# Optimization experiments

Hardware: AMD Instinct MI355X
Metric: run time of the kernel (lower is better)

Reference implementation:

```python
import jax, jax.numpy as jnp
import numpy as np

N = 100000      # nodes
E = 600000      # directed edges (reciprocal pairs)
D_NODE = 128    # node feature dim (== hidden, required by torch.where broadcast)
D_BOND = 16     # bond feature dim
HID = 128       # hidden size
DEPTH = 3       # message passing depth


def setup_inputs() -> dict:
    key = jax.random.key(0)
    ks = jax.random.split(key, 8)
    x = jax.random.normal(ks[0], (N, D_NODE), jnp.float32)
    # build edges as reciprocal pairs: edge 2i = (u,v), edge 2i+1 = (v,u)
    half = E // 2
    u = jax.random.randint(ks[1], (half,), 0, N)
    v = jax.random.randint(ks[2], (half,), 0, N)
    src = jnp.stack([u, v], axis=1).reshape(-1)
    dst = jnp.stack([v, u], axis=1).reshape(-1)
    edge_index = jnp.stack([src, dst])          # [2, E]
    rev_edge_index = jnp.arange(E) ^ 1           # reverse edge of 2i is 2i+1
    edge_attr = jax.random.normal(ks[3], (E, D_BOND), jnp.float32)
    # learned params (Linear: y = x @ W + b)
    s_i = 1.0 / np.sqrt(D_NODE + D_BOND)
    s_h = 1.0 / np.sqrt(HID)
    s_o = 1.0 / np.sqrt(D_NODE + HID)
    W_i = jax.random.normal(ks[4], (D_NODE + D_BOND, HID), jnp.float32) * s_i
    b_i = jnp.zeros((HID,), jnp.float32)
    W_h = jax.random.normal(ks[5], (HID, HID), jnp.float32) * s_h
    b_h = jnp.zeros((HID,), jnp.float32)
    W_o = jax.random.normal(ks[6], (D_NODE + HID, HID), jnp.float32) * s_o
    b_o = jnp.zeros((HID,), jnp.float32)
    return dict(x=x, edge_attr=edge_attr, W_i=W_i, b_i=b_i, W_h=W_h, b_h=b_h,
                W_o=W_o, b_o=b_o, edge_index=edge_index,
                rev_edge_index=rev_edge_index)


def reference(x, edge_attr, W_i, b_i, W_h, b_h, W_o, b_o,
              edge_index, rev_edge_index):
    src, dst = edge_index[0], edge_index[1]
    # H_0 = relu(W_i([x[src]; edge_attr]))
    H0 = jax.nn.relu(jnp.concatenate([x[src], edge_attr], axis=1) @ W_i + b_i)
    H = H0
    for _ in range(DEPTH - 1):
        # message: scatter-sum over dst, gather by src, subtract reverse edge
        agg = jax.ops.segment_sum(H, dst, num_segments=N)   # [N, HID]
        M = agg[src] - H[rev_edge_index]                    # [E, HID]
        # update: relu(H0 + W_h(M))   (dropout is identity in eval)
        H = jax.nn.relu(H0 + M @ W_h + b_h)
    # final node aggregation
    Mn = jax.ops.segment_sum(H, dst, num_segments=N)        # [N, HID]
    Mn = jnp.where(jnp.sum(Mn, axis=1, keepdims=True) == 0, x, Mn)
    out = jax.nn.relu(jnp.concatenate([x, Mn], axis=1) @ W_o + b_o)  # [N, HID]
    return out
```

## Files before the change

kernel.cpp:

```cpp
#include <hip/hip_runtime.h>
#include <hip/hip_bf16.h>

#define N_NODES 100000
#define N_EDGES 600000
#define HID 128
#define D_BOND 16
#define NB_CHUNKS 98

typedef __attribute__((ext_vector_type(8))) short bf16x8;
typedef __attribute__((ext_vector_type(4))) float f32x4;

__device__ __forceinline__ float bf2f(unsigned int u) {
    return __uint_as_float((u & 0xffffu) << 16);
}
__device__ __forceinline__ unsigned short f2bf(float f) {
    unsigned int x = __float_as_uint(f);
    x += 0x7fffu + ((x >> 16) & 1u);
    return (unsigned short)(x >> 16);
}
__device__ __forceinline__ unsigned int pk2(float a, float b) {
    return (unsigned int)f2bf(a) | ((unsigned int)f2bf(b) << 16);
}

__device__ __forceinline__ void st16(unsigned char* tile, int row, int u, uint4 v) {
    *reinterpret_cast<uint4*>(tile + ((row * 512 + u * 16) ^ ((row & 7) << 4))) = v;
}
__device__ __forceinline__ uint4 ld16(const unsigned char* tile, int row, int u) {
    return *reinterpret_cast<const uint4*>(tile + ((row * 512 + u * 16) ^ ((row & 7) << 4)));
}
__device__ __forceinline__ bf16x8 ld_a(const unsigned char* tile, int row, int kbyte) {
    return *reinterpret_cast<const bf16x8*>(tile + ((row * 512 + kbyte) ^ ((row & 7) << 4)));
}
__device__ __forceinline__ void st2(unsigned char* tile, int row, int col, unsigned short v) {
    *reinterpret_cast<unsigned short*>(tile + ((row * 512 + col * 2) ^ ((row & 7) << 4))) = v;
}

template<int NK>
__device__ __forceinline__ void gemm_frag(const unsigned char* tile, const unsigned short* Wp,
                                          int wr, int cb, int l, f32x4 (&acc)[4]) {
    const int arow = 16 * wr + (l & 15);
    const int abyte0 = (l >> 4) * 16;
#pragma unroll
    for (int kk = 0; kk < NK; ++kk) {
        const bf16x8 a = ld_a(tile, arow, kk * 64 + abyte0);
#pragma unroll
        for (int c = 0; c < 4; ++c) {
            const bf16x8 b = *reinterpret_cast<const bf16x8*>(&Wp[(((kk * 8) + cb + c) * 64 + l) * 8]);
            acc[c] = __builtin_amdgcn_mfma_f32_16x16x32_bf16(a, b, acc[c], 0, 0, 0);
        }
    }
}

template<int NK>
__device__ __forceinline__ void gemm_frag2(const unsigned char* tile, const unsigned short* Wp,
                                           int wr0, int cb, int l, f32x4 (&acc)[2][4]) {
    const int abyte0 = (l >> 4) * 16;
    const int ar0 = 16 * wr0 + (l & 15);
#pragma unroll
    for (int kk = 0; kk < NK; ++kk) {
        const bf16x8 a0 = ld_a(tile, ar0, kk * 64 + abyte0);
        const bf16x8 a1 = ld_a(tile, ar0 + 16, kk * 64 + abyte0);
#pragma unroll
        for (int c = 0; c < 4; ++c) {
            const bf16x8 b = *reinterpret_cast<const bf16x8*>(&Wp[(((kk * 8) + cb + c) * 64 + l) * 8]);
            acc[0][c] = __builtin_amdgcn_mfma_f32_16x16x32_bf16(a0, b, acc[0][c], 0, 0, 0);
            acc[1][c] = __builtin_amdgcn_mfma_f32_16x16x32_bf16(a1, b, acc[1][c], 0, 0, 0);
        }
    }
}

__device__ __forceinline__ void epilogue_store(unsigned char* tile,
                                               f32x4 (&acc)[2][4],
                                               const float* __restrict__ bias,
                                               unsigned short* __restrict__ Hdst,
                                               int e0, int wr0, int cb, int l, int t) {
#pragma unroll
    for (int r = 0; r < 2; ++r) {
        const int rbase = 16 * (wr0 + r) + 4 * (l >> 4);
#pragma unroll
        for (int c = 0; c < 4; ++c) {
            const int col = ((cb + c) << 4) | (l & 15);
            const float bv = bias[col];
#pragma unroll
            for (int rr = 0; rr < 4; ++rr)
                st2(tile, rbase + rr, col, f2bf(fmaxf(acc[r][c][rr] + bv, 0.f)));
        }
    }
    __syncthreads();
#pragma unroll
    for (int i = 0; i < 4; ++i) {
        const int f = t + 256 * i;
        const int row = f >> 4, u = f & 15;
        *reinterpret_cast<uint4*>(&Hdst[(size_t)(e0 + row) * HID + u * 8]) = ld16(tile, row, u);
    }
}

__global__ __launch_bounds__(256) void k_hist(const int* __restrict__ dst,
                                              int* __restrict__ cnt) {
    int e = blockIdx.x * 256 + threadIdx.x;
    if (e < N_EDGES) atomicAdd(&cnt[dst[e]], 1);
}

__global__ __launch_bounds__(256) void k_blocksum(const int* __restrict__ cnt,
                                                  int* __restrict__ bsum) {
    __shared__ int red[256];
    const int b = blockIdx.x, t = threadIdx.x;
    const int base = b * 1024 + t * 4;
    int s = 0;
#pragma unroll
    for (int i = 0; i < 4; ++i) { int n = base + i; if (n < N_NODES) s += cnt[n]; }
    red[t] = s; __syncthreads();
    for (int o = 128; o > 0; o >>= 1) { if (t < o) red[t] += red[t + o]; __syncthreads(); }
    if (t == 0) bsum[b] = red[0];
}

__global__ __launch_bounds__(128) void k_scan_bsum(const int* __restrict__ bsum,
                                                   int* __restrict__ boff,
                                                   int* __restrict__ rowptr) {
    __shared__ int s[128];
    const int t = threadIdx.x;
    const int v = (t < NB_CHUNKS) ? bsum[t] : 0;
    s[t] = v; __syncthreads();
    for (int o = 1; o < 128; o <<= 1) {
        int add = 0; if (t >= o) add = s[t - o];
        __syncthreads();
        s[t] += add; __syncthreads();
    }
    if (t < NB_CHUNKS) boff[t] = s[t] - v;
    if (t == 0) rowptr[N_NODES] = N_EDGES;
}

__global__ __launch_bounds__(256) void k_scan_chunk(const int* __restrict__ cnt,
                                                    const int* __restrict__ boff,
                                                    int* __restrict__ rowptr,
                                                    int* __restrict__ wpos) {
    __shared__ int s[256];
    const int b = blockIdx.x, t = threadIdx.x;
    const int base = b * 1024 + t * 4;
    int v[4]; int ts = 0;
#pragma unroll
    for (int i = 0; i < 4; ++i) { int n = base + i; v[i] = (n < N_NODES) ? cnt[n] : 0; ts += v[i]; }
    s[t] = ts; __syncthreads();
    for (int o = 1; o < 256; o <<= 1) {
        int add = 0; if (t >= o) add = s[t - o];
        __syncthreads();
        s[t] += add; __syncthreads();
    }
    int run = s[t] - ts + boff[b];
#pragma unroll
    for (int i = 0; i < 4; ++i) {
        int n = base + i;
        if (n < N_NODES) { rowptr[n] = run; wpos[n] = run; }
        run += v[i];
    }
}

__global__ __launch_bounds__(256) void k_fill(const int* __restrict__ dst,
                                              int* __restrict__ wpos,
                                              int* __restrict__ eidx) {
    int e = blockIdx.x * 256 + threadIdx.x;
    if (e < N_EDGES) { int p = atomicAdd(&wpos[dst[e]], 1); eidx[p] = e; }
}

__global__ __launch_bounds__(256) void k_xcvt(const float* __restrict__ x,
                                              unsigned short* __restrict__ xbf) {
    const size_t i = (size_t)(blockIdx.x * 256 + threadIdx.x) * 8;
    const float4 v0 = *reinterpret_cast<const float4*>(&x[i]);
    const float4 v1 = *reinterpret_cast<const float4*>(&x[i + 4]);
    uint4 o;
    o.x = pk2(v0.x, v0.y); o.y = pk2(v0.z, v0.w);
    o.z = pk2(v1.x, v1.y); o.w = pk2(v1.z, v1.w);
    *reinterpret_cast<uint4*>(&xbf[i]) = o;
}

__global__ __launch_bounds__(256) void k_pack(const float* __restrict__ Wi,
                                              const float* __restrict__ Wh,
                                              const float* __restrict__ Wo,
                                              unsigned short* __restrict__ Pi,
                                              unsigned short* __restrict__ Ph,
                                              unsigned short* __restrict__ PhN,
                                              unsigned short* __restrict__ Po) {
    const int tid = blockIdx.x * 256 + threadIdx.x;
    const float* W; unsigned short* P; int Krows, base; float sgn = 1.f;
    if (tid < 2560)      { W = Wi; P = Pi;  Krows = 144; base = tid; }
    else if (tid < 4608) { W = Wh; P = Ph;  Krows = 128; base = tid - 2560; }
    else if (tid < 6656) { W = Wh; P = PhN; Krows = 128; base = tid - 4608; sgn = -1.f; }
    else                 { W = Wo; P = Po;  Krows = 256; base = tid - 6656; }
    const int l = base & 63, fc = base >> 6;
    const int c = fc & 7, kk = fc >> 3;
    const int col = c * 16 + (l & 15);
    const int k0 = kk * 32 + (l >> 4) * 8;
    float v[8];
#pragma unroll
    for (int j = 0; j < 8; ++j) {
        const int k = k0 + j;
        v[j] = (k < Krows) ? sgn * W[(size_t)k * HID + col] : 0.f;
    }
    uint4 o;
    o.x = pk2(v[0], v[1]); o.y = pk2(v[2], v[3]);
    o.z = pk2(v[4], v[5]); o.w = pk2(v[6], v[7]);
    *reinterpret_cast<uint4*>(&P[(size_t)base * 8]) = o;
}

__device__ __forceinline__ void stage_xe64(unsigned char* tile, const unsigned short* __restrict__ xbf,
                                           const float* __restrict__ ea, const int* s_src,
                                           int e0, int t) {
#pragma unroll
    for (int f = t; f < 1024; f += 256) {
        const int e = f >> 4, u = f & 15;
        const uint4 v = *reinterpret_cast<const uint4*>(&xbf[(size_t)s_src[e] * HID + u * 8]);
        st16(tile, e, u, v);
    }
    if (t < 128) {
        const int e = t >> 1, u = t & 1;
        const float* ep = &ea[(size_t)(e0 + e) * D_BOND + u * 8];
        const float4 v0 = *reinterpret_cast<const float4*>(ep);
        const float4 v1 = *reinterpret_cast<const float4*>(ep + 4);
        uint4 o;
        o.x = pk2(v0.x, v0.y); o.y = pk2(v0.z, v0.w);
        o.z = pk2(v1.x, v1.y); o.w = pk2(v1.z, v1.w);
        st16(tile, e, 16 + u, o);
    } else {
        const int i = t - 128, e = i >> 1, u = i & 1;
        st16(tile, e, 18 + u, make_uint4(0, 0, 0, 0));
    }
}

__global__ __launch_bounds__(256) void k_h0(const unsigned short* __restrict__ xbf,
                                            const float* __restrict__ ea,
                                            const unsigned short* __restrict__ Pi,
                                            const float* __restrict__ bi,
                                            const int* __restrict__ src,
                                            unsigned short* __restrict__ H) {
    __shared__ __align__(16) unsigned char tile[64 * 512];
    __shared__ int s_src[64];
    const int e0 = blockIdx.x * 64;
    const int t = threadIdx.x;
    if (t < 64) s_src[t] = src[e0 + t];
    __syncthreads();
    stage_xe64(tile, xbf, ea, s_src, e0, t);
    __syncthreads();
    const int w = t >> 6, l = t & 63;
    const int cb = (w & 1) * 4, wr0 = (w >> 1) * 2;
    f32x4 acc[2][4] = {};
    gemm_frag2<5>(tile, Pi, wr0, cb, l, acc);
    __syncthreads();
    epilogue_store(tile, acc, bi, H, e0, wr0, cb, l, t);
}

__global__ __launch_bounds__(256) void k_agg(const unsigned short* __restrict__ H,
                                             const int* __restrict__ rowptr,
                                             const int* __restrict__ eidx,
                                             void* __restrict__ aggv) {
    const int wid = (blockIdx.x * 256 + threadIdx.x) >> 6;
    const int lane = threadIdx.x & 63;
    if (wid >= N_NODES) return;
    const int beg = rowptr[wid], end = rowptr[wid + 1];
    float a0 = 0.f, a1 = 0.f;
    int j = beg;
    for (; j + 4 <= end; j += 4) {
        const int ei0 = eidx[j], ei1 = eidx[j + 1], ei2 = eidx[j + 2], ei3 = eidx[j + 3];
        const unsigned int p0 = *reinterpret_cast<const unsigned int*>(&H[(size_t)ei0 * HID + lane * 2]);
        const unsigned int p1 = *reinterpret_cast<const unsigned int*>(&H[(size_t)ei1 * HID + lane * 2]);
        const unsigned int p2 = *reinterpret_cast<const unsigned int*>(&H[(size_t)ei2 * HID + lane * 2]);
        const unsigned int p3 = *reinterpret_cast<const unsigned int*>(&H[(size_t)ei3 * HID + lane * 2]);
        a0 += bf2f(p0) + bf2f(p1) + bf2f(p2) + bf2f(p3);
        a1 += bf2f(p0 >> 16) + bf2f(p1 >> 16) + bf2f(p2 >> 16) + bf2f(p3 >> 16);
    }
    for (; j < end; ++j) {
        const int e = eidx[j];
        const unsigned int p = *reinterpret_cast<const unsigned int*>(&H[(size_t)e * HID + lane * 2]);
        a0 += bf2f(p);
        a1 += bf2f(p >> 16);
    }
    *reinterpret_cast<unsigned int*>((char*)aggv + (size_t)wid * 512 + lane * 4) = pk2(a0, a1);
}

__global__ __launch_bounds__(256) void k_msg(const unsigned short* __restrict__ xbf,
                                             const float* __restrict__ ea,
                                             const void* __restrict__ aggv,
                                             const unsigned short* __restrict__ Pi,
                                             const float* __restrict__ bi,
                                             const unsigned short* __restrict__ Ph,
                                             const unsigned short* __restrict__ PhN,
                                             const float* __restrict__ bh,
                                             const int* __restrict__ src,
                                             unsigned short* H) {
    __shared__ __align__(16) unsigned char tile[64 * 512];
    __shared__ int s_src[64];
    const int e0 = blockIdx.x * 64;
    const int t = threadIdx.x;
    if (t < 64) s_src[t] = src[e0 + t];
    __syncthreads();
    const int w = t >> 6, l = t & 63;
    const int cb = (w & 1) * 4, wr0 = (w >> 1) * 2;

    stage_xe64(tile, xbf, ea, s_src, e0, t);
    __syncthreads();
    f32x4 acc[2][4] = {};
    gemm_frag2<5>(tile, Pi, wr0, cb, l, acc);
#pragma unroll
    for (int r = 0; r < 2; ++r)
#pragma unroll
        for (int c = 0; c < 4; ++c) {
            const float bv = bi[((cb + c) << 4) | (l & 15)];
#pragma unroll
            for (int rr = 0; rr < 4; ++rr) acc[r][c][rr] = fmaxf(acc[r][c][rr] + bv, 0.f);
        }
    __syncthreads();

#pragma unroll
    for (int f = t; f < 1024; f += 256) {
        const int e = f >> 4, u = f & 15;
        st16(tile, e, u,
             *reinterpret_cast<const uint4*>((const char*)aggv + (size_t)s_src[e] * 512 + u * 16));
    }
    __syncthreads();
    gemm_frag2<4>(tile, Ph, wr0, cb, l, acc);
    __syncthreads();

#pragma unroll
    for (int f = t; f < 1024; f += 256) {
        const int e = f >> 4, u = f & 15;
        st16(tile, e, u,
             *reinterpret_cast<const uint4*>(&H[(size_t)((e0 + e) ^ 1) * HID + u * 8]));
    }
    __syncthreads();
    gemm_frag2<4>(tile, PhN, wr0, cb, l, acc);
    __syncthreads();

    epilogue_store(tile, acc, bh, H, e0, wr0, cb, l, t);
}

__global__ __launch_bounds__(256) void k_out(const float* __restrict__ x,
                                             const void* aggv,
                                             const int* __restrict__ cnt,
                                             const unsigned short* __restrict__ Po,
                                             const float* __restrict__ bo,
                                             float* out) {
    __shared__ __align__(16) unsigned char tile[32 * 512];
    __shared__ int s_cnt[32];
    const int n0 = blockIdx.x * 32;
    const int t = threadIdx.x;
    if (t < 32) s_cnt[t] = cnt[n0 + t];
    __syncthreads();
    for (int f = t; f < 1024; f += 256) {
        const int e = f >> 5, u = f & 31;
        uint4 o;
        if (u >= 16 && s_cnt[e] > 0) {
            o = *reinterpret_cast<const uint4*>((const char*)aggv + (size_t)(n0 + e) * 512 + (u - 16) * 16);
        } else {
            const int k8 = (u & 15) * 8;
            const float* xp = &x[(size_t)(n0 + e) * HID + k8];
            const float4 v0 = *reinterpret_cast<const float4*>(xp);
            const float4 v1 = *reinterpret_cast<const float4*>(xp + 4);
            o.x = pk2(v0.x, v0.y); o.y = pk2(v0.z, v0.w);
            o.z = pk2(v1.x, v1.y); o.w = pk2(v1.z, v1.w);
        }
        st16(tile, e, u, o);
    }
    __syncthreads();
    const int w = t >> 6, l = t & 63;
    const int wr = w & 1, cb = (w >> 1) * 4;
    f32x4 acc[4] = {};
    gemm_frag<8>(tile, Po, wr, cb, l, acc);
    const int frow = 16 * wr + 4 * (l >> 4);
#pragma unroll
    for (int c = 0; c < 4; ++c) {
        const int col = ((cb + c) << 4) | (l & 15);
        const float bias = bo[col];
#pragma unroll
        for (int r = 0; r < 4; ++r) {
            out[(size_t)(n0 + frow + r) * HID + col] = fmaxf(acc[c][r] + bias, 0.f);
        }
    }
}

extern "C" void kernel_launch(void* const* d_in, const int* in_sizes, int n_in,
                              void* d_out, int out_size, void* d_ws, size_t ws_size,
                              hipStream_t stream) {
    const float* x  = (const float*)d_in[0];
    const float* ea = (const float*)d_in[1];
    const float* Wi = (const float*)d_in[2];
    const float* bi = (const float*)d_in[3];
    const float* Wh = (const float*)d_in[4];
    const float* bh = (const float*)d_in[5];
    const float* Wo = (const float*)d_in[6];
    const float* bo = (const float*)d_in[7];
    const int* ei   = (const int*)d_in[8];
    const int* src  = ei;
    const int* dst  = ei + N_EDGES;

    char* ws = (char*)d_ws;
    size_t off = 0;
    auto alloc = [&](size_t bytes) -> void* {
        void* p = ws + off;
        off += (bytes + 255) & ~(size_t)255;
        return p;
    };
    unsigned short* H  = (unsigned short*)alloc((size_t)N_EDGES * HID * 2);
    unsigned short* xbf = (unsigned short*)alloc((size_t)N_NODES * HID * 2);
    int* cnt     = (int*)alloc((size_t)N_NODES * 4);
    int* rowptr  = (int*)alloc((size_t)(N_NODES + 1) * 4);
    int* wpos    = (int*)alloc((size_t)N_NODES * 4);
    int* bsum    = (int*)alloc(512);
    int* boff    = (int*)alloc(512);
    int* eidx    = (int*)alloc((size_t)N_EDGES * 4);
    unsigned short* Pi  = (unsigned short*)alloc(2560 * 8 * 2);
    unsigned short* Ph  = (unsigned short*)alloc(2048 * 8 * 2);
    unsigned short* PhN = (unsigned short*)alloc(2048 * 8 * 2);
    unsigned short* Po  = (unsigned short*)alloc(4096 * 8 * 2);
    void* agg = d_out;

    const int EB = (N_EDGES + 255) / 256;

    hipMemsetAsync(cnt, 0, (size_t)N_NODES * 4, stream);
    k_hist<<<EB, 256, 0, stream>>>(dst, cnt);
    k_blocksum<<<NB_CHUNKS, 256, 0, stream>>>(cnt, bsum);
    k_scan_bsum<<<1, 128, 0, stream>>>(bsum, boff, rowptr);
    k_scan_chunk<<<NB_CHUNKS, 256, 0, stream>>>(cnt, boff, rowptr, wpos);
    k_fill<<<EB, 256, 0, stream>>>(dst, wpos, eidx);

    k_xcvt<<<6250, 256, 0, stream>>>(x, xbf);
    k_pack<<<42, 256, 0, stream>>>(Wi, Wh, Wo, Pi, Ph, PhN, Po);

    k_h0<<<N_EDGES / 64, 256, 0, stream>>>(xbf, ea, Pi, bi, src, H);

    k_agg<<<N_NODES / 4, 256, 0, stream>>>(H, rowptr, eidx, agg);
    k_msg<<<N_EDGES / 64, 256, 0, stream>>>(xbf, ea, agg, Pi, bi, Ph, PhN, bh, src, H);

    k_agg<<<N_NODES / 4, 256, 0, stream>>>(H, rowptr, eidx, agg);
    k_msg<<<N_EDGES / 64, 256, 0, stream>>>(xbf, ea, agg, Pi, bi, Ph, PhN, bh, src, H);

    k_agg<<<N_NODES / 4, 256, 0, stream>>>(H, rowptr, eidx, agg);
    k_out<<<N_NODES / 32, 256, 0, stream>>>(x, agg, cnt, Po, bo, (float*)d_out);
}
```

Before: 685.6 us.

## Precompute per-node x@W_i and interleave with aggregate for single gather per edge

Instead of gathering bf16 x per edge and running a K=144 GEMM for H0 in every edge kernel, a new node-level kernel computes x@W_i[:128] once per node and stores it in bf16 alongside the aggregate in one 512-byte row. The edge kernels then gather that combined row once. They inject the precomputed projection into the accumulators through identity-matrix MFMAs, and run only a K=16 GEMM for the bond features, which are now pre-converted to bf16. k_msg also stages all operands in one phase rather than three sequential stage/GEMM rounds, cutting barriers at the cost of more shared memory. Rounding x@W_i to bf16 before adding adds a small precision loss.

```diff
diff --git a/kernel.cpp b/kernel.cpp
--- a/kernel.cpp
+++ b/kernel.cpp
@@ -22,77 +22,30 @@
     return (unsigned int)f2bf(a) | ((unsigned int)f2bf(b) << 16);
 }
 
-__device__ __forceinline__ void st16(unsigned char* tile, int row, int u, uint4 v) {
-    *reinterpret_cast<uint4*>(tile + ((row * 512 + u * 16) ^ ((row & 7) << 4))) = v;
-}
-__device__ __forceinline__ uint4 ld16(const unsigned char* tile, int row, int u) {
-    return *reinterpret_cast<const uint4*>(tile + ((row * 512 + u * 16) ^ ((row & 7) << 4)));
-}
-__device__ __forceinline__ bf16x8 ld_a(const unsigned char* tile, int row, int kbyte) {
-    return *reinterpret_cast<const bf16x8*>(tile + ((row * 512 + kbyte) ^ ((row & 7) << 4)));
-}
-__device__ __forceinline__ void st2(unsigned char* tile, int row, int col, unsigned short v) {
-    *reinterpret_cast<unsigned short*>(tile + ((row * 512 + col * 2) ^ ((row & 7) << 4))) = v;
-}
-
-template<int NK>
-__device__ __forceinline__ void gemm_frag(const unsigned char* tile, const unsigned short* Wp,
-                                          int wr, int cb, int l, f32x4 (&acc)[4]) {
-    const int arow = 16 * wr + (l & 15);
-    const int abyte0 = (l >> 4) * 16;
-#pragma unroll
-    for (int kk = 0; kk < NK; ++kk) {
-        const bf16x8 a = ld_a(tile, arow, kk * 64 + abyte0);
-#pragma unroll
-        for (int c = 0; c < 4; ++c) {
-            const bf16x8 b = *reinterpret_cast<const bf16x8*>(&Wp[(((kk * 8) + cb + c) * 64 + l) * 8]);
-            acc[c] = __builtin_amdgcn_mfma_f32_16x16x32_bf16(a, b, acc[c], 0, 0, 0);
-        }
-    }
-}
-
-template<int NK>
-__device__ __forceinline__ void gemm_frag2(const unsigned char* tile, const unsigned short* Wp,
-                                           int wr0, int cb, int l, f32x4 (&acc)[2][4]) {
-    const int abyte0 = (l >> 4) * 16;
-    const int ar0 = 16 * wr0 + (l & 15);
-#pragma unroll
-    for (int kk = 0; kk < NK; ++kk) {
-        const bf16x8 a0 = ld_a(tile, ar0, kk * 64 + abyte0);
-        const bf16x8 a1 = ld_a(tile, ar0 + 16, kk * 64 + abyte0);
-#pragma unroll
-        for (int c = 0; c < 4; ++c) {
-            const bf16x8 b = *reinterpret_cast<const bf16x8*>(&Wp[(((kk * 8) + cb + c) * 64 + l) * 8]);
-            acc[0][c] = __builtin_amdgcn_mfma_f32_16x16x32_bf16(a0, b, acc[0][c], 0, 0, 0);
-            acc[1][c] = __builtin_amdgcn_mfma_f32_16x16x32_bf16(a1, b, acc[1][c], 0, 0, 0);
-        }
-    }
-}
-
-__device__ __forceinline__ void epilogue_store(unsigned char* tile,
-                                               f32x4 (&acc)[2][4],
-                                               const float* __restrict__ bias,
-                                               unsigned short* __restrict__ Hdst,
-                                               int e0, int wr0, int cb, int l, int t) {
-#pragma unroll
-    for (int r = 0; r < 2; ++r) {
-        const int rbase = 16 * (wr0 + r) + 4 * (l >> 4);
-#pragma unroll
-        for (int c = 0; c < 4; ++c) {
-            const int col = ((cb + c) << 4) | (l & 15);
-            const float bv = bias[col];
-#pragma unroll
-            for (int rr = 0; rr < 4; ++rr)
-                st2(tile, rbase + rr, col, f2bf(fmaxf(acc[r][c][rr] + bv, 0.f)));
-        }
-    }
-    __syncthreads();
-#pragma unroll
-    for (int i = 0; i < 4; ++i) {
-        const int f = t + 256 * i;
-        const int row = f >> 4, u = f & 15;
-        *reinterpret_cast<uint4*>(&Hdst[(size_t)(e0 + row) * HID + u * 8]) = ld16(tile, row, u);
-    }
+template<int STRIDE, int XM>
+__device__ __forceinline__ void stw(unsigned char* tile, int row, int byte, uint4 v) {
+    *reinterpret_cast<uint4*>(tile + ((row * STRIDE + byte) ^ ((row & XM) << 4))) = v;
+}
+template<int STRIDE, int XM>
+__device__ __forceinline__ uint4 ldw(const unsigned char* tile, int row, int byte) {
+    return *reinterpret_cast<const uint4*>(tile + ((row * STRIDE + byte) ^ ((row & XM) << 4)));
+}
+template<int STRIDE, int XM>
+__device__ __forceinline__ bf16x8 lda(const unsigned char* tile, int row, int byte) {
+    return *reinterpret_cast<const bf16x8*>(tile + ((row * STRIDE + byte) ^ ((row & XM) << 4)));
+}
+template<int STRIDE, int XM>
+__device__ __forceinline__ void st2w(unsigned char* tile, int row, int col, unsigned short v) {
+    *reinterpret_cast<unsigned short*>(tile + ((row * STRIDE + col * 2) ^ ((row & XM) << 4))) = v;
+}
+
+__device__ __forceinline__ bf16x8 ifrag(int l, int shift) {
+    bf16x8 b;
+    const int target = (l & 15) + shift;
+#pragma unroll
+    for (int j = 0; j < 8; ++j)
+        b[j] = (short)((((l >> 4) * 8 + j) == target) ? 0x3F80 : 0);
+    return b;
 }
 
 __global__ __launch_bounds__(256) void k_hist(const int* __restrict__ dst,
@@ -162,30 +115,33 @@
     if (e < N_EDGES) { int p = atomicAdd(&wpos[dst[e]], 1); eidx[p] = e; }
 }
 
-__global__ __launch_bounds__(256) void k_xcvt(const float* __restrict__ x,
-                                              unsigned short* __restrict__ xbf) {
+__global__ __launch_bounds__(256) void k_eacvt(const float* __restrict__ ea,
+                                               unsigned short* __restrict__ eabf) {
     const size_t i = (size_t)(blockIdx.x * 256 + threadIdx.x) * 8;
-    const float4 v0 = *reinterpret_cast<const float4*>(&x[i]);
-    const float4 v1 = *reinterpret_cast<const float4*>(&x[i + 4]);
+    if (i >= (size_t)N_EDGES * D_BOND) return;
+    const float4 v0 = *reinterpret_cast<const float4*>(&ea[i]);
+    const float4 v1 = *reinterpret_cast<const float4*>(&ea[i + 4]);
     uint4 o;
     o.x = pk2(v0.x, v0.y); o.y = pk2(v0.z, v0.w);
     o.z = pk2(v1.x, v1.y); o.w = pk2(v1.z, v1.w);
-    *reinterpret_cast<uint4*>(&xbf[i]) = o;
+    *reinterpret_cast<uint4*>(&eabf[i]) = o;
 }
 
 __global__ __launch_bounds__(256) void k_pack(const float* __restrict__ Wi,
                                               const float* __restrict__ Wh,
                                               const float* __restrict__ Wo,
-                                              unsigned short* __restrict__ Pi,
+                                              unsigned short* __restrict__ Pie,
+                                              unsigned short* __restrict__ Pix,
                                               unsigned short* __restrict__ Ph,
                                               unsigned short* __restrict__ PhN,
                                               unsigned short* __restrict__ Po) {
     const int tid = blockIdx.x * 256 + threadIdx.x;
     const float* W; unsigned short* P; int Krows, base; float sgn = 1.f;
-    if (tid < 2560)      { W = Wi; P = Pi;  Krows = 144; base = tid; }
-    else if (tid < 4608) { W = Wh; P = Ph;  Krows = 128; base = tid - 2560; }
-    else if (tid < 6656) { W = Wh; P = PhN; Krows = 128; base = tid - 4608; sgn = -1.f; }
-    else                 { W = Wo; P = Po;  Krows = 256; base = tid - 6656; }
+    if (tid < 512)        { W = Wi + 128 * HID; P = Pie; Krows = 16;  base = tid; }
+    else if (tid < 2560)  { W = Wi; P = Pix; Krows = 128; base = tid - 512; }
+    else if (tid < 4608)  { W = Wh; P = Ph;  Krows = 128; base = tid - 2560; }
+    else if (tid < 6656)  { W = Wh; P = PhN; Krows = 128; base = tid - 4608; sgn = -1.f; }
+    else                  { W = Wo; P = Po;  Krows = 256; base = tid - 6656; }
     const int l = base & 63, fc = base >> 6;
     const int c = fc & 7, kk = fc >> 3;
     const int col = c * 16 + (l & 15);
@@ -202,56 +158,138 @@
     *reinterpret_cast<uint4*>(&P[(size_t)base * 8]) = o;
 }
 
-__device__ __forceinline__ void stage_xe64(unsigned char* tile, const unsigned short* __restrict__ xbf,
-                                           const float* __restrict__ ea, const int* s_src,
-                                           int e0, int t) {
-#pragma unroll
-    for (int f = t; f < 1024; f += 256) {
-        const int e = f >> 4, u = f & 15;
-        const uint4 v = *reinterpret_cast<const uint4*>(&xbf[(size_t)s_src[e] * HID + u * 8]);
-        st16(tile, e, u, v);
-    }
-    if (t < 128) {
-        const int e = t >> 1, u = t & 1;
-        const float* ep = &ea[(size_t)(e0 + e) * D_BOND + u * 8];
-        const float4 v0 = *reinterpret_cast<const float4*>(ep);
-        const float4 v1 = *reinterpret_cast<const float4*>(ep + 4);
+__global__ __launch_bounds__(256) void k_xw(const float* __restrict__ x,
+                                            const unsigned short* __restrict__ Pix,
+                                            void* __restrict__ xa) {
+    __shared__ __align__(16) unsigned char tX[32 * 256];
+    const int n0 = blockIdx.x * 32;
+    const int t = threadIdx.x;
+#pragma unroll
+    for (int i = 0; i < 2; ++i) {
+        const int f = t + 256 * i, row = f >> 4, u = f & 15;
+        const float* xp = &x[(size_t)(n0 + row) * HID + u * 8];
+        const float4 v0 = *reinterpret_cast<const float4*>(xp);
+        const float4 v1 = *reinterpret_cast<const float4*>(xp + 4);
         uint4 o;
         o.x = pk2(v0.x, v0.y); o.y = pk2(v0.z, v0.w);
         o.z = pk2(v1.x, v1.y); o.w = pk2(v1.z, v1.w);
-        st16(tile, e, 16 + u, o);
-    } else {
-        const int i = t - 128, e = i >> 1, u = i & 1;
-        st16(tile, e, 18 + u, make_uint4(0, 0, 0, 0));
-    }
-}
-
-__global__ __launch_bounds__(256) void k_h0(const unsigned short* __restrict__ xbf,
-                                            const float* __restrict__ ea,
-                                            const unsigned short* __restrict__ Pi,
+        stw<256, 7>(tX, row, u * 16, o);
+    }
+    __syncthreads();
+    const int w = t >> 6, l = t & 63;
+    const int wr = w & 1, cb = (w >> 1) * 4;
+    const int arow = 16 * wr + (l & 15);
+    const int ko = (l >> 4) * 16;
+    f32x4 acc[4] = {};
+#pragma unroll
+    for (int kk = 0; kk < 4; ++kk) {
+        const bf16x8 a = lda<256, 7>(tX, arow, kk * 64 + ko);
+#pragma unroll
+        for (int c = 0; c < 4; ++c) {
+            const bf16x8 b = *reinterpret_cast<const bf16x8*>(&Pix[(((kk * 8) + cb + c) * 64 + l) * 8]);
+            acc[c] = __builtin_amdgcn_mfma_f32_16x16x32_bf16(a, b, acc[c], 0, 0, 0);
+        }
+    }
+    __syncthreads();
+    const int rbase = 16 * wr + 4 * (l >> 4);
+#pragma unroll
+    for (int c = 0; c < 4; ++c) {
+        const int col = ((cb + c) << 4) | (l & 15);
+#pragma unroll
+        for (int rr = 0; rr < 4; ++rr)
+            st2w<256, 7>(tX, rbase + rr, col, f2bf(acc[c][rr]));
+    }
+    __syncthreads();
+#pragma unroll
+    for (int i = 0; i < 2; ++i) {
+        const int f = t + 256 * i, row = f >> 4, u = f & 15;
+        *reinterpret_cast<uint4*>((char*)xa + (size_t)(n0 + row) * 512 + u * 16) =
+            ldw<256, 7>(tX, row, u * 16);
+    }
+}
+
+template<int STRIDE>
+__device__ __forceinline__ void xw_init(const unsigned char* tX, int ar0, int ko,
+                                        int cb, int l, f32x4 (&acc)[2][4]) {
+    const bf16x8 bI0 = ifrag(l, 0), bI1 = ifrag(l, 16);
+    const f32x4 z = {0.f, 0.f, 0.f, 0.f};
+#pragma unroll
+    for (int c = 0; c < 4; ++c) {
+        const int fc = cb + c;
+        const int wb = (fc == 7) ? 192 : 32 * fc;
+        const bf16x8 bI = (fc == 7) ? bI1 : bI0;
+        acc[0][c] = __builtin_amdgcn_mfma_f32_16x16x32_bf16(lda<STRIDE, 7>(tX, ar0, wb + ko), bI, z, 0, 0, 0);
+        acc[1][c] = __builtin_amdgcn_mfma_f32_16x16x32_bf16(lda<STRIDE, 7>(tX, ar0 + 16, wb + ko), bI, z, 0, 0, 0);
+    }
+}
+
+__global__ __launch_bounds__(256) void k_h0(const void* __restrict__ xa,
+                                            const unsigned short* __restrict__ eabf,
+                                            const unsigned short* __restrict__ Pie,
                                             const float* __restrict__ bi,
                                             const int* __restrict__ src,
                                             unsigned short* __restrict__ H) {
-    __shared__ __align__(16) unsigned char tile[64 * 512];
+    __shared__ __align__(16) unsigned char tX[64 * 256];
+    __shared__ __align__(16) unsigned char tE[64 * 64];
     __shared__ int s_src[64];
     const int e0 = blockIdx.x * 64;
     const int t = threadIdx.x;
     if (t < 64) s_src[t] = src[e0 + t];
     __syncthreads();
-    stage_xe64(tile, xbf, ea, s_src, e0, t);
+#pragma unroll
+    for (int i = 0; i < 4; ++i) {
+        const int f = t + 256 * i, e = f >> 4, u = f & 15;
+        stw<256, 7>(tX, e, u * 16,
+            *reinterpret_cast<const uint4*>((const char*)xa + (size_t)s_src[e] * 512 + u * 16));
+    }
+    {
+        const int e = t >> 2, u = t & 3;
+        uint4 v = make_uint4(0, 0, 0, 0);
+        if (u < 2) v = *reinterpret_cast<const uint4*>(&eabf[(size_t)(e0 + e) * D_BOND + u * 8]);
+        stw<64, 3>(tE, e, u * 16, v);
+    }
     __syncthreads();
     const int w = t >> 6, l = t & 63;
     const int cb = (w & 1) * 4, wr0 = (w >> 1) * 2;
-    f32x4 acc[2][4] = {};
-    gemm_frag2<5>(tile, Pi, wr0, cb, l, acc);
-    __syncthreads();
-    epilogue_store(tile, acc, bi, H, e0, wr0, cb, l, t);
+    const int ar0 = 16 * wr0 + (l & 15);
+    const int ko = (l >> 4) * 16;
+    f32x4 acc[2][4];
+    xw_init<256>(tX, ar0, ko, cb, l, acc);
+    {
+        const bf16x8 a0 = lda<64, 3>(tE, ar0, ko);
+        const bf16x8 a1 = lda<64, 3>(tE, ar0 + 16, ko);
+#pragma unroll
+        for (int c = 0; c < 4; ++c) {
+            const bf16x8 b = *reinterpret_cast<const bf16x8*>(&Pie[((cb + c) * 64 + l) * 8]);
+            acc[0][c] = __builtin_amdgcn_mfma_f32_16x16x32_bf16(a0, b, acc[0][c], 0, 0, 0);
+            acc[1][c] = __builtin_amdgcn_mfma_f32_16x16x32_bf16(a1, b, acc[1][c], 0, 0, 0);
+        }
+    }
+    __syncthreads();
+#pragma unroll
+    for (int r = 0; r < 2; ++r) {
+        const int rbase = 16 * (wr0 + r) + 4 * (l >> 4);
+#pragma unroll
+        for (int c = 0; c < 4; ++c) {
+            const int col = ((cb + c) << 4) | (l & 15);
+            const float bv = bi[col];
+#pragma unroll
+            for (int rr = 0; rr < 4; ++rr)
+                st2w<256, 7>(tX, rbase + rr, col, f2bf(fmaxf(acc[r][c][rr] + bv, 0.f)));
+        }
+    }
+    __syncthreads();
+#pragma unroll
+    for (int i = 0; i < 4; ++i) {
+        const int f = t + 256 * i, row = f >> 4, u = f & 15;
+        *reinterpret_cast<uint4*>(&H[(size_t)(e0 + row) * HID + u * 8]) = ldw<256, 7>(tX, row, u * 16);
+    }
 }
 
 __global__ __launch_bounds__(256) void k_agg(const unsigned short* __restrict__ H,
                                              const int* __restrict__ rowptr,
                                              const int* __restrict__ eidx,
-                                             void* __restrict__ aggv) {
+                                             void* __restrict__ xa) {
     const int wid = (blockIdx.x * 256 + threadIdx.x) >> 6;
     const int lane = threadIdx.x & 63;
     if (wid >= N_NODES) return;
@@ -273,32 +311,64 @@
         a0 += bf2f(p);
         a1 += bf2f(p >> 16);
     }
-    *reinterpret_cast<unsigned int*>((char*)aggv + (size_t)wid * 512 + lane * 4) = pk2(a0, a1);
-}
-
-__global__ __launch_bounds__(256) void k_msg(const unsigned short* __restrict__ xbf,
-                                             const float* __restrict__ ea,
-                                             const void* __restrict__ aggv,
-                                             const unsigned short* __restrict__ Pi,
+    *reinterpret_cast<unsigned int*>((char*)xa + (size_t)wid * 512 + 256 + lane * 4) = pk2(a0, a1);
+}
+
+__global__ __launch_bounds__(256) void k_msg(const void* __restrict__ xa,
+                                             const unsigned short* __restrict__ eabf,
+                                             const unsigned short* __restrict__ Pie,
                                              const float* __restrict__ bi,
                                              const unsigned short* __restrict__ Ph,
                                              const unsigned short* __restrict__ PhN,
                                              const float* __restrict__ bh,
                                              const int* __restrict__ src,
                                              unsigned short* H) {
-    __shared__ __align__(16) unsigned char tile[64 * 512];
+    __shared__ __align__(16) unsigned char tA[64 * 512];
+    __shared__ __align__(16) unsigned char tH[64 * 256];
+    __shared__ __align__(16) unsigned char tE[64 * 64];
     __shared__ int s_src[64];
     const int e0 = blockIdx.x * 64;
     const int t = threadIdx.x;
     if (t < 64) s_src[t] = src[e0 + t];
     __syncthreads();
+
+#pragma unroll
+    for (int i = 0; i < 8; ++i) {
+        const int f = t + 256 * i, e = f >> 5, u = f & 31;
+        stw<512, 7>(tA, e, u * 16,
+            *reinterpret_cast<const uint4*>((const char*)xa + (size_t)s_src[e] * 512 + u * 16));
+    }
+#pragma unroll
+    for (int i = 0; i < 4; ++i) {
+        const int f = t + 256 * i, e = f >> 4, u = f & 15;
+        stw<256, 7>(tH, e, u * 16,
+            *reinterpret_cast<const uint4*>(&H[(size_t)((e0 + e) ^ 1) * HID + u * 8]));
+    }
+    {
+        const int e = t >> 2, u = t & 3;
+        uint4 v = make_uint4(0, 0, 0, 0);
+        if (u < 2) v = *reinterpret_cast<const uint4*>(&eabf[(size_t)(e0 + e) * D_BOND + u * 8]);
+        stw<64, 3>(tE, e, u * 16, v);
+    }
+    __syncthreads();
+
     const int w = t >> 6, l = t & 63;
     const int cb = (w & 1) * 4, wr0 = (w >> 1) * 2;
-
-    stage_xe64(tile, xbf, ea, s_src, e0, t);
-    __syncthreads();
-    f32x4 acc[2][4] = {};
-    gemm_frag2<5>(tile, Pi, wr0, cb, l, acc);
+    const int ar0 = 16 * wr0 + (l & 15);
+    const int ko = (l >> 4) * 16;
+
+    f32x4 acc[2][4];
+    xw_init<512>(tA, ar0, ko, cb, l, acc);
+    {
+        const bf16x8 a0 = lda<64, 3>(tE, ar0, ko);
+        const bf16x8 a1 = lda<64, 3>(tE, ar0 + 16, ko);
+#pragma unroll
+        for (int c = 0; c < 4; ++c) {
+            const bf16x8 b = *reinterpret_cast<const bf16x8*>(&Pie[((cb + c) * 64 + l) * 8]);
+            acc[0][c] = __builtin_amdgcn_mfma_f32_16x16x32_bf16(a0, b, acc[0][c], 0, 0, 0);
+            acc[1][c] = __builtin_amdgcn_mfma_f32_16x16x32_bf16(a1, b, acc[1][c], 0, 0, 0);
+        }
+    }
 #pragma unroll
     for (int r = 0; r < 2; ++r)
 #pragma unroll
@@ -307,33 +377,52 @@
 #pragma unroll
             for (int rr = 0; rr < 4; ++rr) acc[r][c][rr] = fmaxf(acc[r][c][rr] + bv, 0.f);
         }
-    __syncthreads();
-
-#pragma unroll
-    for (int f = t; f < 1024; f += 256) {
-        const int e = f >> 4, u = f & 15;
-        st16(tile, e, u,
-             *reinterpret_cast<const uint4*>((const char*)aggv + (size_t)s_src[e] * 512 + u * 16));
-    }
-    __syncthreads();
-    gemm_frag2<4>(tile, Ph, wr0, cb, l, acc);
-    __syncthreads();
-
-#pragma unroll
-    for (int f = t; f < 1024; f += 256) {
-        const int e = f >> 4, u = f & 15;
-        st16(tile, e, u,
-             *reinterpret_cast<const uint4*>(&H[(size_t)((e0 + e) ^ 1) * HID + u * 8]));
-    }
-    __syncthreads();
-    gemm_frag2<4>(tile, PhN, wr0, cb, l, acc);
-    __syncthreads();
-
-    epilogue_store(tile, acc, bh, H, e0, wr0, cb, l, t);
+#pragma unroll
+    for (int kk = 0; kk < 4; ++kk) {
+        const bf16x8 a0 = lda<512, 7>(tA, ar0, 256 + kk * 64 + ko);
+        const bf16x8 a1 = lda<512, 7>(tA, ar0 + 16, 256 + kk * 64 + ko);
+#pragma unroll
+        for (int c = 0; c < 4; ++c) {
+            const bf16x8 b = *reinterpret_cast<const bf16x8*>(&Ph[(((kk * 8) + cb + c) * 64 + l) * 8]);
+            acc[0][c] = __builtin_amdgcn_mfma_f32_16x16x32_bf16(a0, b, acc[0][c], 0, 0, 0);
+            acc[1][c] = __builtin_amdgcn_mfma_f32_16x16x32_bf16(a1, b, acc[1][c], 0, 0, 0);
+        }
+    }
+#pragma unroll
+    for (int kk = 0; kk < 4; ++kk) {
+        const bf16x8 a0 = lda<256, 7>(tH, ar0, kk * 64 + ko);
+        const bf16x8 a1 = lda<256, 7>(tH, ar0 + 16, kk * 64 + ko);
+#pragma unroll
+        for (int c = 0; c < 4; ++c) {
+            const bf16x8 b = *reinterpret_cast<const bf16x8*>(&PhN[(((kk * 8) + cb + c) * 64 + l) * 8]);
+            acc[0][c] = __builtin_amdgcn_mfma_f32_16x16x32_bf16(a0, b, acc[0][c], 0, 0, 0);
+            acc[1][c] = __builtin_amdgcn_mfma_f32_16x16x32_bf16(a1, b, acc[1][c], 0, 0, 0);
+        }
+    }
+    __syncthreads();
+
+#pragma unroll
+    for (int r = 0; r < 2; ++r) {
+        const int rbase = 16 * (wr0 + r) + 4 * (l >> 4);
+#pragma unroll
+        for (int c = 0; c < 4; ++c) {
+            const int col = ((cb + c) << 4) | (l & 15);
+            const float bv = bh[col];
+#pragma unroll
+            for (int rr = 0; rr < 4; ++rr)
+                st2w<256, 7>(tH, rbase + rr, col, f2bf(fmaxf(acc[r][c][rr] + bv, 0.f)));
+        }
+    }
+    __syncthreads();
+#pragma unroll
+    for (int i = 0; i < 4; ++i) {
+        const int f = t + 256 * i, row = f >> 4, u = f & 15;
+        *reinterpret_cast<uint4*>(&H[(size_t)(e0 + row) * HID + u * 8]) = ldw<256, 7>(tH, row, u * 16);
+    }
 }
 
 __global__ __launch_bounds__(256) void k_out(const float* __restrict__ x,
-                                             const void* aggv,
+                                             const void* xa,
                                              const int* __restrict__ cnt,
                                              const unsigned short* __restrict__ Po,
                                              const float* __restrict__ bo,
@@ -348,7 +437,7 @@
         const int e = f >> 5, u = f & 31;
         uint4 o;
         if (u >= 16 && s_cnt[e] > 0) {
-            o = *reinterpret_cast<const uint4*>((const char*)aggv + (size_t)(n0 + e) * 512 + (u - 16) * 16);
+            o = *reinterpret_cast<const uint4*>((const char*)xa + (size_t)(n0 + e) * 512 + 256 + (u - 16) * 16);
         } else {
             const int k8 = (u & 15) * 8;
             const float* xp = &x[(size_t)(n0 + e) * HID + k8];
@@ -357,13 +446,23 @@
             o.x = pk2(v0.x, v0.y); o.y = pk2(v0.z, v0.w);
             o.z = pk2(v1.x, v1.y); o.w = pk2(v1.z, v1.w);
         }
-        st16(tile, e, u, o);
+        stw<512, 7>(tile, e, u * 16, o);
     }
     __syncthreads();
     const int w = t >> 6, l = t & 63;
     const int wr = w & 1, cb = (w >> 1) * 4;
+    const int arow = 16 * wr + (l & 15);
+    const int ko = (l >> 4) * 16;
     f32x4 acc[4] = {};
-    gemm_frag<8>(tile, Po, wr, cb, l, acc);
+#pragma unroll
+    for (int kk = 0; kk < 8; ++kk) {
+        const bf16x8 a = lda<512, 7>(tile, arow, kk * 64 + ko);
+#pragma unroll
+        for (int c = 0; c < 4; ++c) {
+            const bf16x8 b = *reinterpret_cast<const bf16x8*>(&Po[(((kk * 8) + cb + c) * 64 + l) * 8]);
+            acc[c] = __builtin_amdgcn_mfma_f32_16x16x32_bf16(a, b, acc[c], 0, 0, 0);
+        }
+    }
     const int frow = 16 * wr + 4 * (l >> 4);
 #pragma unroll
     for (int c = 0; c < 4; ++c) {
@@ -398,19 +497,20 @@
         off += (bytes + 255) & ~(size_t)255;
         return p;
     };
-    unsigned short* H  = (unsigned short*)alloc((size_t)N_EDGES * HID * 2);
-    unsigned short* xbf = (unsigned short*)alloc((size_t)N_NODES * HID * 2);
+    unsigned short* H    = (unsigned short*)alloc((size_t)N_EDGES * HID * 2);
+    unsigned short* eabf = (unsigned short*)alloc((size_t)N_EDGES * D_BOND * 2);
     int* cnt     = (int*)alloc((size_t)N_NODES * 4);
     int* rowptr  = (int*)alloc((size_t)(N_NODES + 1) * 4);
     int* wpos    = (int*)alloc((size_t)N_NODES * 4);
     int* bsum    = (int*)alloc(512);
     int* boff    = (int*)alloc(512);
     int* eidx    = (int*)alloc((size_t)N_EDGES * 4);
-    unsigned short* Pi  = (unsigned short*)alloc(2560 * 8 * 2);
+    unsigned short* Pie = (unsigned short*)alloc(512 * 8 * 2);
+    unsigned short* Pix = (unsigned short*)alloc(2048 * 8 * 2);
     unsigned short* Ph  = (unsigned short*)alloc(2048 * 8 * 2);
     unsigned short* PhN = (unsigned short*)alloc(2048 * 8 * 2);
     unsigned short* Po  = (unsigned short*)alloc(4096 * 8 * 2);
-    void* agg = d_out;
+    void* xa = d_out;
 
     const int EB = (N_EDGES + 255) / 256;
 
@@ -421,17 +521,18 @@
     k_scan_chunk<<<NB_CHUNKS, 256, 0, stream>>>(cnt, boff, rowptr, wpos);
     k_fill<<<EB, 256, 0, stream>>>(dst, wpos, eidx);
 
-    k_xcvt<<<6250, 256, 0, stream>>>(x, xbf);
-    k_pack<<<42, 256, 0, stream>>>(Wi, Wh, Wo, Pi, Ph, PhN, Po);
-
-    k_h0<<<N_EDGES / 64, 256, 0, stream>>>(xbf, ea, Pi, bi, src, H);
-
-    k_agg<<<N_NODES / 4, 256, 0, stream>>>(H, rowptr, eidx, agg);
-    k_msg<<<N_EDGES / 64, 256, 0, stream>>>(xbf, ea, agg, Pi, bi, Ph, PhN, bh, src, H);
-
-    k_agg<<<N_NODES / 4, 256, 0, stream>>>(H, rowptr, eidx, agg);
-    k_msg<<<N_EDGES / 64, 256, 0, stream>>>(xbf, ea, agg, Pi, bi, Ph, PhN, bh, src, H);
-
-    k_agg<<<N_NODES / 4, 256, 0, stream>>>(H, rowptr, eidx, agg);
-    k_out<<<N_NODES / 32, 256, 0, stream>>>(x, agg, cnt, Po, bo, (float*)d_out);
-}
+    k_eacvt<<<(N_EDGES * D_BOND / 8 + 255) / 256, 256, 0, stream>>>(ea, eabf);
+    k_pack<<<42, 256, 0, stream>>>(Wi, Wh, Wo, Pie, Pix, Ph, PhN, Po);
+    k_xw<<<N_NODES / 32, 256, 0, stream>>>(x, Pix, xa);
+
+    k_h0<<<N_EDGES / 64, 256, 0, stream>>>(xa, eabf, Pie, bi, src, H);
+
+    k_agg<<<N_NODES / 4, 256, 0, stream>>>(H, rowptr, eidx, xa);
+    k_msg<<<N_EDGES / 64, 256, 0, stream>>>(xa, eabf, Pie, bi, Ph, PhN, bh, src, H);
+
+    k_agg<<<N_NODES / 4, 256, 0, stream>>>(H, rowptr, eidx, xa);
+    k_msg<<<N_EDGES / 64, 256, 0, stream>>>(xa, eabf, Pie, bi, Ph, PhN, bh, src, H);
+
+    k_agg<<<N_NODES / 4, 256, 0, stream>>>(H, rowptr, eidx, xa);
+    k_out<<<N_NODES / 32, 256, 0, stream>>>(x, xa, cnt, Po, bo, (float*)d_out);
+}
```

After: 625.8 us, median of 4. 8.7% less time.
